# Kernel optimization log

Measured on AMD Instinct MI355X. Metric: run time of the kernel, lower is better.

The kernel has to match this reference:

```python
import jax, jax.numpy as jnp
import numpy as np

TOPK_RATIO = 0.2
ALIGN_WEIGHT = 1.0
REG_WEIGHT = 0.1
EPS_LN = 1e-6
EPS_COS = 1e-8


def setup_inputs() -> dict:
    key = jax.random.key(0)
    k1, k2, k3, k4, k5 = jax.random.split(key, 5)
    B, C, H, W = 8, 256, 200, 200
    return {
        "bev_map": jax.random.normal(k1, (B, C, H, W), dtype=jnp.float32),
        "prior_warp": jax.random.normal(k2, (B, C, H, W), dtype=jnp.float32),
        "dx_m": jax.random.normal(k3, (B,), dtype=jnp.float32),
        "dy_m": jax.random.normal(k4, (B,), dtype=jnp.float32),
        "dtheta": jax.random.normal(k5, (B,), dtype=jnp.float32),
    }


def _channel_layer_norm(x):
    # per-pixel mean/std over channel dim; torch std is unbiased (ddof=1)
    mu = jnp.mean(x, axis=1, keepdims=True)
    sigma = jnp.std(x, axis=1, keepdims=True, ddof=1) + EPS_LN
    return (x - mu) / sigma


def reference(bev_map, prior_warp, dx_m, dy_m, dtheta):
    B, C, H, W = bev_map.shape
    bev_norm = _channel_layer_norm(bev_map)      # [B,C,H,W]
    prior_norm = _channel_layer_norm(prior_warp)  # [B,C,H,W]

    # squared-sum score per pixel, flattened over spatial dims
    score = jnp.sum(bev_map * bev_map, axis=1).reshape(B, H * W)  # [B,HW]
    k = max(1, int(TOPK_RATIO * H * W))
    _, idx = jax.lax.top_k(score, k)             # [B,k]

    idx_bc = jnp.broadcast_to(idx[:, None, :], (B, C, k))
    bev_topk = jnp.take_along_axis(bev_norm.reshape(B, C, H * W), idx_bc, axis=2)
    prior_topk = jnp.take_along_axis(prior_norm.reshape(B, C, H * W), idx_bc, axis=2)

    # cosine similarity over channel dim (torch eps semantics: clamp each norm)
    num = jnp.sum(bev_topk * prior_topk, axis=1)                       # [B,k]
    na = jnp.sqrt(jnp.sum(bev_topk * bev_topk, axis=1))
    nb = jnp.sqrt(jnp.sum(prior_topk * prior_topk, axis=1))
    sim = num / (jnp.maximum(na, EPS_COS) * jnp.maximum(nb, EPS_COS))
    align_loss = jnp.mean(1.0 - sim)

    reg_loss = jnp.mean(dx_m * dx_m + dy_m * dy_m) + jnp.mean(dtheta * dtheta)
    return ALIGN_WEIGHT * align_loss + REG_WEIGHT * reg_loss
```

## Files before the change

### kernel.cpp

```cpp
#include <hip/hip_runtime.h>
#include <math.h>

#define BATCH 8
#define CCH 256
#define HW 40000
#define HW4 (HW / 4)
#define KSEL 8000
#define EPS_LN 1e-6f
#define EPS_COS 1e-8f
#define SLICES 40
#define SLICE_LEN (HW / SLICES)

#define OFF_SCORE   0
#define OFF_CONTRIB 320000
#define OFF_HIST1   640000
#define OFF_HIST2   1164288
#define OFF_PREFIX  1688576
#define OFF_REM1    1688584
#define OFF_TKEY    1688592
#define OFF_REM2    1688600
#define OFF_TIE     1688608
#define OFF_BSUMS   1688616

__device__ __forceinline__ unsigned int mono_key(float x) {
  unsigned int u = __float_as_uint(x);
  return (u & 0x80000000u) ? ~u : (u | 0x80000000u);
}

__global__ __launch_bounds__(256) void zero_kernel(unsigned int* __restrict__ ws) {
  const int n4 = (2 * BATCH * 65536) / 4;
  uint4* p = (uint4*)(ws + OFF_HIST1);
  uint4 z = {0u, 0u, 0u, 0u};
  for (int i = blockIdx.x * blockDim.x + threadIdx.x; i < n4; i += gridDim.x * blockDim.x)
    p[i] = z;
  if (blockIdx.x == 0 && threadIdx.x < BATCH) ws[OFF_BSUMS + threadIdx.x] = 0u;
}

__global__ __launch_bounds__(256) void pixel_stats_kernel(
    const float* __restrict__ A, const float* __restrict__ B,
    float* __restrict__ score, float* __restrict__ contrib) {
  int tid = blockIdx.x * blockDim.x + threadIdx.x;
  if (tid >= BATCH * HW4) return;
  int b = tid / HW4;
  int p4 = tid - b * HW4;
  const float4* a  = (const float4*)(A + (size_t)b * CCH * HW) + p4;
  const float4* bb = (const float4*)(B + (size_t)b * CCH * HW) + p4;

  float sa[4] = {0, 0, 0, 0}, ssa[4] = {0, 0, 0, 0};
  float sb[4] = {0, 0, 0, 0}, ssb[4] = {0, 0, 0, 0}, dab[4] = {0, 0, 0, 0};
#pragma unroll 4
  for (int c = 0; c < CCH; ++c) {
    float4 x = a[(size_t)c * HW4];
    float4 y = bb[(size_t)c * HW4];
    float xs[4] = {x.x, x.y, x.z, x.w};
    float ys[4] = {y.x, y.y, y.z, y.w};
#pragma unroll
    for (int j = 0; j < 4; ++j) {
      sa[j] += xs[j];
      ssa[j] = fmaf(xs[j], xs[j], ssa[j]);
      sb[j] += ys[j];
      ssb[j] = fmaf(ys[j], ys[j], ssb[j]);
      dab[j] = fmaf(xs[j], ys[j], dab[j]);
    }
  }

  float scv[4], cov[4];
  const float invC = 1.0f / (float)CCH;
#pragma unroll
  for (int j = 0; j < 4; ++j) {
    scv[j] = ssa[j];
    float mua = sa[j] * invC, mub = sb[j] * invC;
    float cssa = fmaxf(ssa[j] - (float)CCH * mua * mua, 0.f);
    float cssb = fmaxf(ssb[j] - (float)CCH * mub * mub, 0.f);
    float cdot = dab[j] - (float)CCH * mua * mub;
    float siga = sqrtf(cssa / (float)(CCH - 1)) + EPS_LN;
    float sigb = sqrtf(cssb / (float)(CCH - 1)) + EPS_LN;
    float num = cdot / (siga * sigb);
    float na = sqrtf(cssa) / siga;
    float nb = sqrtf(cssb) / sigb;
    cov[j] = 1.0f - num / (fmaxf(na, EPS_COS) * fmaxf(nb, EPS_COS));
  }
  int out = b * HW + p4 * 4;
  *(float4*)(score + out)   = make_float4(scv[0], scv[1], scv[2], scv[3]);
  *(float4*)(contrib + out) = make_float4(cov[0], cov[1], cov[2], cov[3]);
}

__global__ __launch_bounds__(256) void hist1_kernel(
    const float* __restrict__ score, unsigned int* __restrict__ ws) {
  int b = blockIdx.x / SLICES;
  int sl = blockIdx.x - b * SLICES;
  const float* s = score + b * HW;
  unsigned int* h = ws + OFF_HIST1 + (b << 16);
  int base = sl * SLICE_LEN;
  for (int i = base + threadIdx.x; i < base + SLICE_LEN; i += 256) {
    unsigned int key = mono_key(s[i]);
    atomicAdd(&h[key >> 16], 1u);
  }
}

__global__ __launch_bounds__(256) void hist2_kernel(
    const float* __restrict__ score, unsigned int* __restrict__ ws) {
  int b = blockIdx.x / SLICES;
  int sl = blockIdx.x - b * SLICES;
  const float* s = score + b * HW;
  unsigned int pref = ws[OFF_PREFIX + b];
  unsigned int* h = ws + OFF_HIST2 + (b << 16);
  int base = sl * SLICE_LEN;
  for (int i = base + threadIdx.x; i < base + SLICE_LEN; i += 256) {
    unsigned int key = mono_key(s[i]);
    if ((key >> 16) == pref) atomicAdd(&h[key & 0xFFFFu], 1u);
  }
}

__global__ __launch_bounds__(1024) void select_kernel(unsigned int* __restrict__ ws,
                                                      int phase) {
  int b = blockIdx.x;
  const unsigned int* h = ws + (phase ? OFF_HIST2 : OFF_HIST1) + (b << 16);
  unsigned int K = phase ? ws[OFF_REM1 + b] : (unsigned int)KSEL;

  __shared__ unsigned int chunk[1024];
  __shared__ unsigned int suf[1024];
  __shared__ unsigned int s_chunk_idx, s_cum_above;
  __shared__ unsigned int bins[64];

  int t = threadIdx.x;
  unsigned int sum = 0;
#pragma unroll 8
  for (int i = 0; i < 64; ++i) sum += h[t * 64 + i];
  chunk[t] = sum;
  suf[t] = sum;
  __syncthreads();
  for (int off = 1; off < 1024; off <<= 1) {
    unsigned int v = (t + off < 1024) ? suf[t + off] : 0u;
    __syncthreads();
    suf[t] += v;
    __syncthreads();
  }
  unsigned int above = (t == 1023) ? 0u : suf[t + 1];
  if (suf[t] >= K && above < K) { s_chunk_idx = (unsigned int)t; s_cum_above = above; }
  __syncthreads();
  if (t < 64) bins[t] = h[s_chunk_idx * 64 + t];
  __syncthreads();
  if (t == 0) {
    unsigned int cum = s_cum_above;
    int d = 63;
    for (; d >= 0; --d) {
      if (cum + bins[d] >= K) break;
      cum += bins[d];
    }
    unsigned int binidx = s_chunk_idx * 64 + (unsigned int)d;
    if (phase == 0) {
      ws[OFF_PREFIX + b] = binidx;
      ws[OFF_REM1 + b] = K - cum;
    } else {
      ws[OFF_TKEY + b] = (ws[OFF_PREFIX + b] << 16) | binidx;
      ws[OFF_REM2 + b] = K - cum;
      ws[OFF_TIE + b] = 0u;
    }
  }
}

__global__ __launch_bounds__(256) void sum_kernel(
    const float* __restrict__ score, const float* __restrict__ contrib,
    unsigned int* __restrict__ ws) {
  int b = blockIdx.x / SLICES;
  int sl = blockIdx.x - b * SLICES;
  const float* s = score + b * HW;
  const float* ct = contrib + b * HW;
  unsigned int T = ws[OFF_TKEY + b];
  unsigned int rem2 = ws[OFF_REM2 + b];

  float partial = 0.f;
  int base = sl * SLICE_LEN;
  for (int i = base + threadIdx.x; i < base + SLICE_LEN; i += 256) {
    unsigned int key = mono_key(s[i]);
    if (key > T) {
      partial += ct[i];
    } else if (key == T) {
      unsigned int old = atomicAdd(&ws[OFF_TIE + b], 1u);
      if (old < rem2) partial += ct[i];
    }
  }

  __shared__ float red[256];
  red[threadIdx.x] = partial;
  __syncthreads();
  for (int off = 128; off > 0; off >>= 1) {
    if (threadIdx.x < (unsigned)off) red[threadIdx.x] += red[threadIdx.x + off];
    __syncthreads();
  }
  if (threadIdx.x == 0) atomicAdd((float*)(ws + OFF_BSUMS) + b, red[0]);
}

__global__ void finalize_kernel(const unsigned int* __restrict__ ws,
                                const float* __restrict__ dx,
                                const float* __restrict__ dy,
                                const float* __restrict__ dth,
                                float* __restrict__ out) {
  if (threadIdx.x == 0 && blockIdx.x == 0) {
    const float* bsums = (const float*)(ws + OFF_BSUMS);
    float s = 0.f;
    for (int b = 0; b < BATCH; ++b) s += bsums[b];
    float align = s / (float)(BATCH * KSEL);
    float r1 = 0.f, r2 = 0.f;
    for (int b = 0; b < BATCH; ++b) {
      r1 += dx[b] * dx[b] + dy[b] * dy[b];
      r2 += dth[b] * dth[b];
    }
    out[0] = align + 0.1f * (r1 / (float)BATCH + r2 / (float)BATCH);
  }
}

extern "C" void kernel_launch(void* const* d_in, const int* in_sizes, int n_in,
                              void* d_out, int out_size, void* d_ws, size_t ws_size,
                              hipStream_t stream) {
  const float* bev   = (const float*)d_in[0];
  const float* prior = (const float*)d_in[1];
  const float* dx    = (const float*)d_in[2];
  const float* dy    = (const float*)d_in[3];
  const float* dth   = (const float*)d_in[4];
  float* out = (float*)d_out;

  unsigned int* ws = (unsigned int*)d_ws;
  float* score   = (float*)ws + OFF_SCORE;
  float* contrib = (float*)ws + OFF_CONTRIB;

  zero_kernel<<<256, 256, 0, stream>>>(ws);
  pixel_stats_kernel<<<(BATCH * HW4 + 255) / 256, 256, 0, stream>>>(bev, prior, score, contrib);
  hist1_kernel<<<BATCH * SLICES, 256, 0, stream>>>(score, ws);
  select_kernel<<<BATCH, 1024, 0, stream>>>(ws, 0);
  hist2_kernel<<<BATCH * SLICES, 256, 0, stream>>>(score, ws);
  select_kernel<<<BATCH, 1024, 0, stream>>>(ws, 1);
  sum_kernel<<<BATCH * SLICES, 256, 0, stream>>>(score, contrib, ws);
  finalize_kernel<<<1, 64, 0, stream>>>(ws, dx, dy, dth, out);
}
```

Measured before the change: 714.8 us.

## Split channel reduction across warps and fuse histogram and finalize kernels

The per-pixel stats kernel now splits the 256 channels into four slices handled by separate 64-thread groups, combining partial sums through shared memory. This gives more parallelism and more loads in flight for the memory-bound pass. The first histogram pass is folded into the stats kernel, and the finalize step runs in the last block of the sum kernel using a done counter. This removes two launches and one reread of the score array, at the cost of extra shared memory traffic and a fence-plus-atomic completion pattern.

Result: no change. 728.2 us (+1.9%).

```diff
diff --git a/kernel.cpp b/kernel.cpp
--- a/kernel.cpp
+++ b/kernel.cpp
@@ -10,6 +10,9 @@
 #define EPS_COS 1e-8f
 #define SLICES 40
 #define SLICE_LEN (HW / SLICES)
+#define CSLICE 4
+#define CPS (CCH / CSLICE)
+#define BPB 157
 
 #define OFF_SCORE   0
 #define OFF_CONTRIB 320000
@@ -21,6 +24,7 @@
 #define OFF_REM2    1688600
 #define OFF_TIE     1688608
 #define OFF_BSUMS   1688616
+#define OFF_DONE    1688624
 
 __device__ __forceinline__ unsigned int mono_key(float x) {
   unsigned int u = __float_as_uint(x);
@@ -33,68 +37,78 @@
   uint4 z = {0u, 0u, 0u, 0u};
   for (int i = blockIdx.x * blockDim.x + threadIdx.x; i < n4; i += gridDim.x * blockDim.x)
     p[i] = z;
-  if (blockIdx.x == 0 && threadIdx.x < BATCH) ws[OFF_BSUMS + threadIdx.x] = 0u;
-}
-
-__global__ __launch_bounds__(256) void pixel_stats_kernel(
+  if (blockIdx.x == 0 && threadIdx.x < 17) ws[OFF_TIE + threadIdx.x] = 0u;
+}
+
+__global__ __launch_bounds__(256) void stats_kernel(
     const float* __restrict__ A, const float* __restrict__ B,
-    float* __restrict__ score, float* __restrict__ contrib) {
-  int tid = blockIdx.x * blockDim.x + threadIdx.x;
-  if (tid >= BATCH * HW4) return;
-  int b = tid / HW4;
-  int p4 = tid - b * HW4;
-  const float4* a  = (const float4*)(A + (size_t)b * CCH * HW) + p4;
-  const float4* bb = (const float4*)(B + (size_t)b * CCH * HW) + p4;
-
-  float sa[4] = {0, 0, 0, 0}, ssa[4] = {0, 0, 0, 0};
-  float sb[4] = {0, 0, 0, 0}, ssb[4] = {0, 0, 0, 0}, dab[4] = {0, 0, 0, 0};
+    float* __restrict__ score, float* __restrict__ contrib,
+    unsigned int* __restrict__ ws) {
+  __shared__ float sm[CSLICE][20][64];
+  int b = blockIdx.x / BPB;
+  int blk = blockIdx.x - b * BPB;
+  int pix = threadIdx.x & 63;
+  int slice = threadIdx.x >> 6;
+  int p4 = blk * 64 + pix;
+  bool active = p4 < HW4;
+
+  float acc[20];
+#pragma unroll
+  for (int m = 0; m < 20; ++m) acc[m] = 0.f;
+
+  if (active) {
+    const float4* a  = (const float4*)A + ((size_t)b * CCH + slice * CPS) * HW4 + p4;
+    const float4* bb = (const float4*)B + ((size_t)b * CCH + slice * CPS) * HW4 + p4;
 #pragma unroll 4
-  for (int c = 0; c < CCH; ++c) {
-    float4 x = a[(size_t)c * HW4];
-    float4 y = bb[(size_t)c * HW4];
-    float xs[4] = {x.x, x.y, x.z, x.w};
-    float ys[4] = {y.x, y.y, y.z, y.w};
+    for (int c = 0; c < CPS; ++c) {
+      float4 x = a[(size_t)c * HW4];
+      float4 y = bb[(size_t)c * HW4];
+      float xs[4] = {x.x, x.y, x.z, x.w};
+      float ys[4] = {y.x, y.y, y.z, y.w};
+#pragma unroll
+      for (int j = 0; j < 4; ++j) {
+        acc[0 * 4 + j] += xs[j];
+        acc[1 * 4 + j] = fmaf(xs[j], xs[j], acc[1 * 4 + j]);
+        acc[2 * 4 + j] += ys[j];
+        acc[3 * 4 + j] = fmaf(ys[j], ys[j], acc[3 * 4 + j]);
+        acc[4 * 4 + j] = fmaf(xs[j], ys[j], acc[4 * 4 + j]);
+      }
+    }
+  }
+#pragma unroll
+  for (int m = 0; m < 20; ++m) sm[slice][m][pix] = acc[m];
+  __syncthreads();
+
+  if (slice == 0 && active) {
+    float v[20];
+#pragma unroll
+    for (int m = 0; m < 20; ++m)
+      v[m] = sm[0][m][pix] + sm[1][m][pix] + sm[2][m][pix] + sm[3][m][pix];
+
+    float scv[4], cov[4];
+    const float invC = 1.0f / (float)CCH;
 #pragma unroll
     for (int j = 0; j < 4; ++j) {
-      sa[j] += xs[j];
-      ssa[j] = fmaf(xs[j], xs[j], ssa[j]);
-      sb[j] += ys[j];
-      ssb[j] = fmaf(ys[j], ys[j], ssb[j]);
-      dab[j] = fmaf(xs[j], ys[j], dab[j]);
-    }
-  }
-
-  float scv[4], cov[4];
-  const float invC = 1.0f / (float)CCH;
-#pragma unroll
-  for (int j = 0; j < 4; ++j) {
-    scv[j] = ssa[j];
-    float mua = sa[j] * invC, mub = sb[j] * invC;
-    float cssa = fmaxf(ssa[j] - (float)CCH * mua * mua, 0.f);
-    float cssb = fmaxf(ssb[j] - (float)CCH * mub * mub, 0.f);
-    float cdot = dab[j] - (float)CCH * mua * mub;
-    float siga = sqrtf(cssa / (float)(CCH - 1)) + EPS_LN;
-    float sigb = sqrtf(cssb / (float)(CCH - 1)) + EPS_LN;
-    float num = cdot / (siga * sigb);
-    float na = sqrtf(cssa) / siga;
-    float nb = sqrtf(cssb) / sigb;
-    cov[j] = 1.0f - num / (fmaxf(na, EPS_COS) * fmaxf(nb, EPS_COS));
-  }
-  int out = b * HW + p4 * 4;
-  *(float4*)(score + out)   = make_float4(scv[0], scv[1], scv[2], scv[3]);
-  *(float4*)(contrib + out) = make_float4(cov[0], cov[1], cov[2], cov[3]);
-}
-
-__global__ __launch_bounds__(256) void hist1_kernel(
-    const float* __restrict__ score, unsigned int* __restrict__ ws) {
-  int b = blockIdx.x / SLICES;
-  int sl = blockIdx.x - b * SLICES;
-  const float* s = score + b * HW;
-  unsigned int* h = ws + OFF_HIST1 + (b << 16);
-  int base = sl * SLICE_LEN;
-  for (int i = base + threadIdx.x; i < base + SLICE_LEN; i += 256) {
-    unsigned int key = mono_key(s[i]);
-    atomicAdd(&h[key >> 16], 1u);
+      float sa = v[0 * 4 + j], ssa = v[1 * 4 + j];
+      float sb = v[2 * 4 + j], ssb = v[3 * 4 + j], dab = v[4 * 4 + j];
+      scv[j] = ssa;
+      float mua = sa * invC, mub = sb * invC;
+      float cssa = fmaxf(ssa - (float)CCH * mua * mua, 0.f);
+      float cssb = fmaxf(ssb - (float)CCH * mub * mub, 0.f);
+      float cdot = dab - (float)CCH * mua * mub;
+      float siga = sqrtf(cssa / (float)(CCH - 1)) + EPS_LN;
+      float sigb = sqrtf(cssb / (float)(CCH - 1)) + EPS_LN;
+      float num = cdot / (siga * sigb);
+      float na = sqrtf(cssa) / siga;
+      float nb = sqrtf(cssb) / sigb;
+      cov[j] = 1.0f - num / (fmaxf(na, EPS_COS) * fmaxf(nb, EPS_COS));
+    }
+    int out = b * HW + p4 * 4;
+    *(float4*)(score + out)   = make_float4(scv[0], scv[1], scv[2], scv[3]);
+    *(float4*)(contrib + out) = make_float4(cov[0], cov[1], cov[2], cov[3]);
+    unsigned int* h = ws + OFF_HIST1 + (b << 16);
+#pragma unroll
+    for (int j = 0; j < 4; ++j) atomicAdd(&h[mono_key(scv[j]) >> 16], 1u);
   }
 }
 
@@ -118,7 +132,6 @@
   const unsigned int* h = ws + (phase ? OFF_HIST2 : OFF_HIST1) + (b << 16);
   unsigned int K = phase ? ws[OFF_REM1 + b] : (unsigned int)KSEL;
 
-  __shared__ unsigned int chunk[1024];
   __shared__ unsigned int suf[1024];
   __shared__ unsigned int s_chunk_idx, s_cum_above;
   __shared__ unsigned int bins[64];
@@ -127,7 +140,6 @@
   unsigned int sum = 0;
 #pragma unroll 8
   for (int i = 0; i < 64; ++i) sum += h[t * 64 + i];
-  chunk[t] = sum;
   suf[t] = sum;
   __syncthreads();
   for (int off = 1; off < 1024; off <<= 1) {
@@ -160,9 +172,11 @@
   }
 }
 
-__global__ __launch_bounds__(256) void sum_kernel(
+__global__ __launch_bounds__(256) void sum_finalize_kernel(
     const float* __restrict__ score, const float* __restrict__ contrib,
-    unsigned int* __restrict__ ws) {
+    unsigned int* __restrict__ ws,
+    const float* __restrict__ dx, const float* __restrict__ dy,
+    const float* __restrict__ dth, float* __restrict__ out) {
   int b = blockIdx.x / SLICES;
   int sl = blockIdx.x - b * SLICES;
   const float* s = score + b * HW;
@@ -189,25 +203,22 @@
     if (threadIdx.x < (unsigned)off) red[threadIdx.x] += red[threadIdx.x + off];
     __syncthreads();
   }
-  if (threadIdx.x == 0) atomicAdd((float*)(ws + OFF_BSUMS) + b, red[0]);
-}
-
-__global__ void finalize_kernel(const unsigned int* __restrict__ ws,
-                                const float* __restrict__ dx,
-                                const float* __restrict__ dy,
-                                const float* __restrict__ dth,
-                                float* __restrict__ out) {
-  if (threadIdx.x == 0 && blockIdx.x == 0) {
-    const float* bsums = (const float*)(ws + OFF_BSUMS);
-    float s = 0.f;
-    for (int b = 0; b < BATCH; ++b) s += bsums[b];
-    float align = s / (float)(BATCH * KSEL);
-    float r1 = 0.f, r2 = 0.f;
-    for (int b = 0; b < BATCH; ++b) {
-      r1 += dx[b] * dx[b] + dy[b] * dy[b];
-      r2 += dth[b] * dth[b];
-    }
-    out[0] = align + 0.1f * (r1 / (float)BATCH + r2 / (float)BATCH);
+  if (threadIdx.x == 0) {
+    atomicAdd((float*)(ws + OFF_BSUMS) + b, red[0]);
+    __threadfence();
+    unsigned int t = atomicAdd(&ws[OFF_DONE], 1u);
+    if (t == BATCH * SLICES - 1) {
+      float ssum = 0.f;
+      for (int i = 0; i < BATCH; ++i)
+        ssum += atomicAdd((float*)(ws + OFF_BSUMS) + i, 0.0f);
+      float align = ssum / (float)(BATCH * KSEL);
+      float r1 = 0.f, r2 = 0.f;
+      for (int i = 0; i < BATCH; ++i) {
+        r1 += dx[i] * dx[i] + dy[i] * dy[i];
+        r2 += dth[i] * dth[i];
+      }
+      out[0] = align + 0.1f * (r1 / (float)BATCH + r2 / (float)BATCH);
+    }
   }
 }
 
@@ -226,11 +237,9 @@
   float* contrib = (float*)ws + OFF_CONTRIB;
 
   zero_kernel<<<256, 256, 0, stream>>>(ws);
-  pixel_stats_kernel<<<(BATCH * HW4 + 255) / 256, 256, 0, stream>>>(bev, prior, score, contrib);
-  hist1_kernel<<<BATCH * SLICES, 256, 0, stream>>>(score, ws);
+  stats_kernel<<<BATCH * BPB, 256, 0, stream>>>(bev, prior, score, contrib, ws);
   select_kernel<<<BATCH, 1024, 0, stream>>>(ws, 0);
   hist2_kernel<<<BATCH * SLICES, 256, 0, stream>>>(score, ws);
   select_kernel<<<BATCH, 1024, 0, stream>>>(ws, 1);
-  sum_kernel<<<BATCH * SLICES, 256, 0, stream>>>(score, contrib, ws);
-  finalize_kernel<<<1, 64, 0, stream>>>(ws, dx, dy, dth, out);
-}
+  sum_finalize_kernel<<<BATCH * SLICES, 256, 0, stream>>>(score, contrib, ws, dx, dy, dth, out);
+}
```
